# Performance work log

Measured on AMD Instinct MI355X. Metric: run time of the kernel, lower is better.

## Reference

```python
import jax, jax.numpy as jnp
import numpy as np

B, S, D, H, PF = 2, 2048, 1024, 16, 4096
HD = D // H
EPS = 1e-5


def _rope_tables(seq_len, dim, theta=10000.0):
    freqs = 1.0 / (theta ** (np.arange(0, dim, 2)[: dim // 2].astype(np.float32) / dim))
    ang = np.outer(np.arange(seq_len, dtype=np.float32), freqs)  # [S, D/2]
    return jnp.asarray(np.cos(ang)), jnp.asarray(np.sin(ang))


def setup_inputs() -> dict:
    key = jax.random.key(0)
    ks = jax.random.split(key, 16)
    s = 0.02
    inp = {
        "src": jax.random.normal(ks[0], (B, S, D), dtype=jnp.float32),
        "Wq": jax.random.normal(ks[1], (D, D), dtype=jnp.float32) * s,
        "bq": jnp.zeros((D,), jnp.float32),
        "Wk": jax.random.normal(ks[2], (D, D), dtype=jnp.float32) * s,
        "bk": jnp.zeros((D,), jnp.float32),
        "Wv": jax.random.normal(ks[3], (D, D), dtype=jnp.float32) * s,
        "bv": jnp.zeros((D,), jnp.float32),
        "Wo": jax.random.normal(ks[4], (D, D), dtype=jnp.float32) * s,
        "bo": jnp.zeros((D,), jnp.float32),
        "ln1_g": jnp.ones((D,), jnp.float32),
        "ln1_b": jnp.zeros((D,), jnp.float32),
        "W1": jax.random.normal(ks[5], (D, PF), dtype=jnp.float32) * s,
        "b1": jnp.zeros((PF,), jnp.float32),
        "W2": jax.random.normal(ks[6], (PF, D), dtype=jnp.float32) * s,
        "b2": jnp.zeros((D,), jnp.float32),
        "ln2_g": jnp.ones((D,), jnp.float32),
        "ln2_b": jnp.zeros((D,), jnp.float32),
    }
    cos, sin = _rope_tables(S, D)
    inp["rope_cos"] = cos
    inp["rope_sin"] = sin
    return inp


def _apply_rope(x, cos, sin):
    # x: [B, S, D]; rotate adjacent channel pairs as complex numbers (Meta LLaMA style)
    xp = x.reshape(x.shape[0], x.shape[1], -1, 2)
    a, b = xp[..., 0], xp[..., 1]
    c = cos[None, : x.shape[1]]
    s = sin[None, : x.shape[1]]
    out = jnp.stack([a * c - b * s, a * s + b * c], axis=-1)
    return out.reshape(x.shape)


def _layer_norm(x, g, b):
    mu = x.mean(-1, keepdims=True)
    var = ((x - mu) ** 2).mean(-1, keepdims=True)
    return (x - mu) * jax.lax.rsqrt(var + EPS) * g + b


def reference(src, Wq, bq, Wk, bk, Wv, bv, Wo, bo, ln1_g, ln1_b,
              W1, b1, W2, b2, ln2_g, ln2_b, rope_cos, rope_sin):
    bsz, seq, _ = src.shape
    Q = src @ Wq + bq
    K = src @ Wk + bk
    V = src @ Wv + bv
    Q = _apply_rope(Q, rope_cos, rope_sin)
    K = _apply_rope(K, rope_cos, rope_sin)
    # split heads: [B, H, S, HD]
    Q = Q.reshape(bsz, seq, H, HD).transpose(0, 2, 1, 3)
    K = K.reshape(bsz, seq, H, HD).transpose(0, 2, 1, 3)
    V = V.reshape(bsz, seq, H, HD).transpose(0, 2, 1, 3)
    scale = 1.0 / jnp.sqrt(jnp.float32(HD))
    energy = jnp.einsum("bhqd,bhkd->bhqk", Q, K) * scale
    attn = jax.nn.softmax(energy, axis=-1)
    x = jnp.einsum("bhqk,bhkd->bhqd", attn, V)
    x = x.transpose(0, 2, 1, 3).reshape(bsz, seq, D)
    attn_out = x @ Wo + bo
    # residual + LayerNorm
    h = _layer_norm(src + attn_out, ln1_g, ln1_b)
    # positionwise feedforward
    ff = jax.nn.relu(h @ W1 + b1) @ W2 + b2
    return _layer_norm(h + ff, ln2_g, ln2_b)
```

## Files before the change

### kernel.cpp

```cpp
#include <hip/hip_runtime.h>

#define SEQ 2048
#define DIM 1024
#define NH 16
#define HDIM 64
#define PFF 4096
#define NROWS 4096
#define BATCH 2
#define NQKV 3072

typedef unsigned short u16;
typedef unsigned int u32;
typedef __attribute__((ext_vector_type(8))) short short8;
typedef __attribute__((ext_vector_type(4))) float f32x4;
typedef __attribute__((ext_vector_type(16))) float f32x16;

__device__ inline float b2f(u16 u){ return __uint_as_float(((u32)u)<<16); }
__device__ inline u16 f2b(float f){
  u32 u = __float_as_uint(f);
  u32 r = u + 0x7FFFu + ((u>>16)&1u);
  return (u16)(r>>16);
}

#define AS1C(p) ((const __attribute__((address_space(1))) unsigned int*)(p))
#define AS3P(p) ((__attribute__((address_space(3))) unsigned int*)(p))

__global__ void k_cast_bf16(const float* __restrict__ in, u16* __restrict__ out, int n4){
  int i = blockIdx.x*256 + threadIdx.x;
  if (i >= n4) return;
  float4 v = ((const float4*)in)[i];
  ushort4 o;
  o.x = f2b(v.x); o.y = f2b(v.y); o.z = f2b(v.z); o.w = f2b(v.w);
  ((ushort4*)out)[i] = o;
}

__global__ __launch_bounds__(256) void k_transpose_cast(const float* __restrict__ in,
                                                        u16* __restrict__ out, int R, int C){
  __shared__ float tile[32][33];
  int tx = threadIdx.x & 31, ty = threadIdx.x >> 5;
  int c0 = blockIdx.x*32, r0 = blockIdx.y*32;
  #pragma unroll
  for (int i=0;i<4;++i)
    tile[ty+i*8][tx] = in[(size_t)(r0+ty+i*8)*C + c0 + tx];
  __syncthreads();
  #pragma unroll
  for (int i=0;i<4;++i)
    out[(size_t)(c0+ty+i*8)*R + r0 + tx] = f2b(tile[tx][ty+i*8]);
}

__global__ __launch_bounds__(256) void k_transpose_v(const u16* __restrict__ QKV, u16* __restrict__ VT){
  __shared__ u16 tile[32][34];
  int tx = threadIdx.x & 31, ty = threadIdx.x >> 5;
  int d0 = blockIdx.x*32, r0 = blockIdx.y*32;
  #pragma unroll
  for (int i=0;i<4;++i)
    tile[ty+i*8][tx] = QKV[(size_t)(r0+ty+i*8)*NQKV + 2048 + d0 + tx];
  __syncthreads();
  #pragma unroll
  for (int i=0;i<4;++i)
    VT[(size_t)(d0+ty+i*8)*NROWS + r0 + tx] = tile[tx][ty+i*8];
}

__global__ void k_pack3(const float* __restrict__ a, const float* __restrict__ b,
                        const float* __restrict__ c, float* __restrict__ o){
  int i = blockIdx.x*256 + threadIdx.x;
  if (i >= NQKV) return;
  o[i] = i < 1024 ? a[i] : (i < 2048 ? b[i-1024] : c[i-2048]);
}

template<bool RELU, bool BF16OUT, bool BIAS>
__global__ __launch_bounds__(256) void k_gemm(
    const u16* __restrict__ A, const u16* __restrict__ Bt,
    const float* __restrict__ bias, void* __restrict__ Cp,
    int M, int N, int Kc, int lda, int ldb){
  __shared__ __align__(16) char lds[32768];
  const int tid = threadIdx.x;
  const int lane = tid & 63, wid = tid >> 6;
  const int quad = lane >> 4, l15 = lane & 15;
  const int wr = wid >> 1, wc = wid & 1;
  const int nwg = gridDim.x * gridDim.y;
  int lid = blockIdx.y * gridDim.x + blockIdx.x;
  lid = (lid & 7) * (nwg >> 3) + (lid >> 3);
  const int bx = lid % gridDim.x, by = lid / gridDim.x;
  const int rowBase = by * 128, colBase = bx * 128;
  const u16* Az = A  + (size_t)blockIdx.z * Kc;
  const u16* Bz = Bt + (size_t)blockIdx.z * Kc;
  f32x4 acc[4][4] = {};
  const int srow = lane >> 3;
  const int scol = lane & 7;
  for (int k0 = 0; k0 < Kc; k0 += 64) {
    __syncthreads();
    #pragma unroll
    for (int i=0;i<4;++i){
      int wch = wid*4 + i;
      int row = wch*8 + srow;
      int c   = scol ^ (row & 7);
      const u16* ga = Az + (size_t)(rowBase+row)*lda + k0 + c*8;
      __builtin_amdgcn_global_load_lds(AS1C(ga), AS3P(lds + wch*1024), 16, 0, 0);
      const u16* gb = Bz + (size_t)(colBase+row)*ldb + k0 + c*8;
      __builtin_amdgcn_global_load_lds(AS1C(gb), AS3P(lds + 16384 + wch*1024), 16, 0, 0);
    }
    __syncthreads();
    #pragma unroll
    for (int kk=0;kk<2;++kk){
      short8 af[4], bfr[4];
      #pragma unroll
      for (int m=0;m<4;++m){
        int r = wr*64 + m*16 + l15;
        af[m] = *(const short8*)(lds + ((r*128 + kk*64 + quad*16) ^ ((r&7)<<4)));
      }
      #pragma unroll
      for (int n=0;n<4;++n){
        int r = wc*64 + n*16 + l15;
        bfr[n] = *(const short8*)(lds + 16384 + ((r*128 + kk*64 + quad*16) ^ ((r&7)<<4)));
      }
      __builtin_amdgcn_s_setprio(1);
      #pragma unroll
      for (int m=0;m<4;++m)
        #pragma unroll
        for (int n=0;n<4;++n)
          acc[m][n] = __builtin_amdgcn_mfma_f32_16x16x32_bf16(af[m], bfr[n], acc[m][n], 0,0,0);
      __builtin_amdgcn_s_setprio(0);
    }
  }
  float* Cf = (float*)Cp + (size_t)blockIdx.z * M * N;
  #pragma unroll
  for (int m=0;m<4;++m){
    #pragma unroll
    for (int n=0;n<4;++n){
      int col = colBase + wc*64 + n*16 + l15;
      float bv = (BIAS && blockIdx.z == 0) ? bias[col] : 0.f;
      #pragma unroll
      for (int j=0;j<4;++j){
        int row = rowBase + wr*64 + m*16 + quad*4 + j;
        float v = acc[m][n][j] + bv;
        if (RELU) v = fmaxf(v, 0.f);
        if (BF16OUT) ((u16*)Cp)[(size_t)row*N + col] = f2b(v);
        else         Cf[(size_t)row*N + col] = v;
      }
    }
  }
}

__global__ void k_rope(u16* __restrict__ QKV,
                       const float* __restrict__ cosT, const float* __restrict__ sinT){
  int idx = blockIdx.x*256 + threadIdx.x;
  int row = idx >> 9, p = idx & 511;
  int s = row & (SEQ-1);
  float c = cosT[s*512 + p], sn = sinT[s*512 + p];
  u16* qp = QKV + (size_t)row*NQKV + 2*p;
  u16* kp = qp + 1024;
  ushort2 q = *(ushort2*)qp;
  ushort2 k = *(ushort2*)kp;
  float qx = b2f(q.x), qy = b2f(q.y), kx = b2f(k.x), ky = b2f(k.y);
  const float scale = 0.125f;
  ushort2 qo, ko;
  qo.x = f2b((qx*c - qy*sn)*scale);
  qo.y = f2b((qx*sn + qy*c)*scale);
  ko.x = f2b(kx*c - ky*sn);
  ko.y = f2b(kx*sn + ky*c);
  *(ushort2*)qp = qo;
  *(ushort2*)kp = ko;
}

__global__ __launch_bounds__(256) void k_attn(
    const u16* __restrict__ QKV, const u16* __restrict__ VT, u16* __restrict__ Xo){
  const int qt = blockIdx.x, h = blockIdx.y, b = blockIdx.z;
  const int tid = threadIdx.x, lane = tid & 63, wid = tid >> 6;
  const int l31 = lane & 31, hi = lane >> 5;
  __shared__ __align__(16) char lds[32768];
  const int srow = lane >> 3, scol = lane & 7;

  short8 qf[4];
  {
    const u16* qrow = QKV + (size_t)(b*SEQ + qt*128 + wid*32 + l31)*NQKV + h*HDIM;
    #pragma unroll
    for (int dk=0; dk<4; ++dk)
      qf[dk] = *(const short8*)(qrow + dk*16 + 8*hi);
  }
  float m_run = -1e30f, s_run = 0.f;
  f32x16 oacc[2] = {};
  const size_t krow0 = (size_t)(b*SEQ);

  auto do_stage = [&](int buf, int kt){
    char* kdst = lds + buf*16384;
    char* vdst = kdst + 8192;
    #pragma unroll
    for (int i=0;i<2;++i){
      int wch = wid*2 + i;
      int row = wch*8 + srow;
      int c = scol ^ (row & 7);
      const u16* gk = QKV + (krow0 + kt*64 + row)*NQKV + 1024 + h*HDIM + c*8;
      __builtin_amdgcn_global_load_lds(AS1C(gk), AS3P(kdst + wch*1024), 16, 0, 0);
      const u16* gv = VT + (size_t)(h*HDIM + row)*NROWS + b*SEQ + kt*64 + c*8;
      __builtin_amdgcn_global_load_lds(AS1C(gv), AS3P(vdst + wch*1024), 16, 0, 0);
    }
  };

  auto do_tile = [&](int buf){
    char* kb = lds + buf*16384;
    char* vb = kb + 8192;
    f32x16 pacc[2] = {};
    __builtin_amdgcn_s_setprio(1);
    #pragma unroll
    for (int kbk=0;kbk<2;++kbk){
      #pragma unroll
      for (int dk=0;dk<4;++dk){
        int row = kbk*32 + l31;
        short8 kf = *(const short8*)(kb + ((row*128 + dk*32 + 16*hi) ^ ((row&7)<<4)));
        pacc[kbk] = __builtin_amdgcn_mfma_f32_32x32x16_bf16(kf, qf[dk], pacc[kbk], 0,0,0);
      }
    }
    __builtin_amdgcn_s_setprio(0);
    float tmax = -1e30f;
    #pragma unroll
    for (int kbk=0;kbk<2;++kbk)
      #pragma unroll
      for (int r=0;r<16;++r) tmax = fmaxf(tmax, pacc[kbk][r]);
    tmax = fmaxf(tmax, __shfl_xor(tmax, 32));
    if (__any(tmax > m_run + 8.0f)){
      float mnew = fmaxf(m_run, tmax);
      float a = __expf(m_run - mnew);
      s_run *= a;
      m_run = mnew;
      #pragma unroll
      for (int r=0;r<16;++r){
        int src = (r&3) + 8*(r>>2) + 4*hi;
        float ar = __shfl(a, src);
        oacc[0][r] *= ar;
        oacc[1][r] *= ar;
      }
    }
    float p[2][16];
    float psum = 0.f;
    #pragma unroll
    for (int kbk=0;kbk<2;++kbk)
      #pragma unroll
      for (int r=0;r<16;++r){
        float e = __expf(pacc[kbk][r] - m_run);
        p[kbk][r] = e;
        psum += e;
      }
    psum += __shfl_xor(psum, 32);
    s_run += psum;
    short8 pa[4];
    #pragma unroll
    for (int kbk=0;kbk<2;++kbk){
      #pragma unroll
      for (int s=0;s<2;++s){
        u32 X0, X1, Y0, Y1;
        asm("v_cvt_pk_bf16_f32 %0, %1, %2" : "=v"(X0) : "v"(p[kbk][8*s+0]), "v"(p[kbk][8*s+1]));
        asm("v_cvt_pk_bf16_f32 %0, %1, %2" : "=v"(X1) : "v"(p[kbk][8*s+2]), "v"(p[kbk][8*s+3]));
        asm("v_cvt_pk_bf16_f32 %0, %1, %2" : "=v"(Y0) : "v"(p[kbk][8*s+4]), "v"(p[kbk][8*s+5]));
        asm("v_cvt_pk_bf16_f32 %0, %1, %2" : "=v"(Y1) : "v"(p[kbk][8*s+6]), "v"(p[kbk][8*s+7]));
        asm volatile("v_permlane32_swap_b32 %0, %1" : "+v"(X0), "+v"(Y0));
        asm volatile("v_permlane32_swap_b32 %0, %1" : "+v"(X1), "+v"(Y1));
        union { u32 w[4]; short8 s8; } pu;
        pu.w[0] = X0; pu.w[1] = X1; pu.w[2] = Y0; pu.w[3] = Y1;
        pa[2*kbk+s] = pu.s8;
      }
    }
    __builtin_amdgcn_s_setprio(1);
    #pragma unroll
    for (int db=0;db<2;++db){
      #pragma unroll
      for (int ks=0;ks<4;++ks){
        int row = db*32 + l31;
        short8 vf = *(const short8*)(vb + ((row*128 + ks*32 + 16*hi) ^ ((row&7)<<4)));
        oacc[db] = __builtin_amdgcn_mfma_f32_32x32x16_bf16(pa[ks], vf, oacc[db], 0,0,0);
      }
    }
    __builtin_amdgcn_s_setprio(0);
  };

  do_stage(0, 0);
  __syncthreads();
  const int NT = SEQ/64;
  #pragma unroll 1
  for (int kt=0; kt<NT; kt+=2){
    do_stage(1, kt+1);
    do_tile(0);
    __syncthreads();
    if (kt+2 < NT) do_stage(0, kt+2);
    do_tile(1);
    __syncthreads();
  }
  #pragma unroll
  for (int r=0;r<16;++r){
    int crow = (r&3) + 8*(r>>2) + 4*hi;
    float sq = __shfl(s_run, crow);
    float rs = __builtin_amdgcn_rcpf(sq);
    int grow = b*SEQ + qt*128 + wid*32 + crow;
    Xo[(size_t)grow*DIM + h*HDIM + l31]      = f2b(oacc[0][r] * rs);
    Xo[(size_t)grow*DIM + h*HDIM + 32 + l31] = f2b(oacc[1][r] * rs);
  }
}

template<int PARTS, bool WBF>
__global__ __launch_bounds__(256) void k_ln(
    const float* __restrict__ a, const float* __restrict__ p0, const float* __restrict__ p1,
    const float* __restrict__ p2, const float* __restrict__ p3,
    const float* __restrict__ g, const float* __restrict__ be,
    float* __restrict__ outf, u16* __restrict__ outb){
  const int row = blockIdx.x, tid = threadIdx.x;
  __shared__ float red[8];
  float4 av = ((const float4*)(a  + (size_t)row*DIM))[tid];
  float4 b0 = ((const float4*)(p0 + (size_t)row*DIM))[tid];
  float4 b1 = ((const float4*)(p1 + (size_t)row*DIM))[tid];
  float x0 = av.x+b0.x+b1.x, x1 = av.y+b0.y+b1.y, x2 = av.z+b0.z+b1.z, x3 = av.w+b0.w+b1.w;
  if constexpr (PARTS == 4){
    float4 b2v = ((const float4*)(p2 + (size_t)row*DIM))[tid];
    float4 b3v = ((const float4*)(p3 + (size_t)row*DIM))[tid];
    x0 += b2v.x+b3v.x; x1 += b2v.y+b3v.y; x2 += b2v.z+b3v.z; x3 += b2v.w+b3v.w;
  }
  float s = x0+x1+x2+x3;
  #pragma unroll
  for (int o=32;o>=1;o>>=1) s += __shfl_down(s, o);
  if ((tid&63)==0) red[tid>>6] = s;
  __syncthreads();
  float mean = (red[0]+red[1]+red[2]+red[3]) * (1.0f/DIM);
  float d0=x0-mean, d1=x1-mean, d2=x2-mean, d3=x3-mean;
  float vs = d0*d0+d1*d1+d2*d2+d3*d3;
  #pragma unroll
  for (int o=32;o>=1;o>>=1) vs += __shfl_down(vs, o);
  if ((tid&63)==0) red[4+(tid>>6)] = vs;
  __syncthreads();
  float var = (red[4]+red[5]+red[6]+red[7]) * (1.0f/DIM);
  float rs = rsqrtf(var + 1e-5f);
  float4 gv = ((const float4*)g)[tid];
  float4 bev = ((const float4*)be)[tid];
  float4 y;
  y.x = d0*rs*gv.x + bev.x;
  y.y = d1*rs*gv.y + bev.y;
  y.z = d2*rs*gv.z + bev.z;
  y.w = d3*rs*gv.w + bev.w;
  ((float4*)(outf + (size_t)row*DIM))[tid] = y;
  if (WBF){
    ushort4 o4; o4.x=f2b(y.x); o4.y=f2b(y.y); o4.z=f2b(y.z); o4.w=f2b(y.w);
    ((ushort4*)(outb + (size_t)row*DIM))[tid] = o4;
  }
}

extern "C" void kernel_launch(void* const* d_in, const int* in_sizes, int n_in,
                              void* d_out, int out_size, void* d_ws, size_t ws_size,
                              hipStream_t stream){
  (void)in_sizes; (void)n_in; (void)out_size; (void)ws_size;
  const float* src  = (const float*)d_in[0];
  const float* Wq   = (const float*)d_in[1];
  const float* bq   = (const float*)d_in[2];
  const float* Wk   = (const float*)d_in[3];
  const float* bk   = (const float*)d_in[4];
  const float* Wv   = (const float*)d_in[5];
  const float* bv   = (const float*)d_in[6];
  const float* Wo   = (const float*)d_in[7];
  const float* bo   = (const float*)d_in[8];
  const float* ln1g = (const float*)d_in[9];
  const float* ln1b = (const float*)d_in[10];
  const float* W1   = (const float*)d_in[11];
  const float* b1   = (const float*)d_in[12];
  const float* W2   = (const float*)d_in[13];
  const float* b2   = (const float*)d_in[14];
  const float* ln2g = (const float*)d_in[15];
  const float* ln2b = (const float*)d_in[16];
  const float* rc   = (const float*)d_in[17];
  const float* rsn  = (const float*)d_in[18];

  char* ws = (char*)d_ws;
  const size_t MB = (size_t)1<<20;
  u16* Xbf   = (u16*)(ws);
  u16* QKV   = (u16*)(ws + 8*MB);
  u16* VTb   = (u16*)(ws + 32*MB);
  float* aop   = (float*)(ws + 8*MB);
  float* ff2p  = (float*)(ws + 8*MB);
  u16* xat   = (u16*)(ws + 40*MB);
  u16* hbf   = (u16*)(ws + 48*MB);
  u16* WqkvT = (u16*)(ws + 56*MB);
  u16* WoT   = (u16*)(ws + 62*MB);
  u16* W1T   = (u16*)(ws + 64*MB);
  u16* W2T   = (u16*)(ws + 72*MB);
  u16* ff1   = (u16*)(ws + 80*MB);
  float* h   = (float*)(ws + 112*MB);
  float* bqkv= (float*)(ws + 128*MB);
  const size_t P16 = 16*MB/4;

  dim3 blk(256);
  k_cast_bf16<<<dim3(NROWS*DIM/1024), blk, 0, stream>>>(src, Xbf, NROWS*DIM/4);
  k_transpose_cast<<<dim3(DIM/32, DIM/32), blk, 0, stream>>>(Wq, WqkvT, DIM, DIM);
  k_transpose_cast<<<dim3(DIM/32, DIM/32), blk, 0, stream>>>(Wk, WqkvT + (size_t)1024*1024, DIM, DIM);
  k_transpose_cast<<<dim3(DIM/32, DIM/32), blk, 0, stream>>>(Wv, WqkvT + (size_t)2048*1024, DIM, DIM);
  k_transpose_cast<<<dim3(DIM/32, DIM/32), blk, 0, stream>>>(Wo, WoT, DIM, DIM);
  k_transpose_cast<<<dim3(PFF/32, DIM/32), blk, 0, stream>>>(W1, W1T, DIM, PFF);
  k_transpose_cast<<<dim3(DIM/32, PFF/32), blk, 0, stream>>>(W2, W2T, PFF, DIM);
  k_pack3<<<dim3(12), blk, 0, stream>>>(bq, bk, bv, bqkv);

  k_gemm<false,true,true><<<dim3(NQKV/128, NROWS/128), blk, 0, stream>>>(
      Xbf, WqkvT, bqkv, QKV, NROWS, NQKV, DIM, DIM, DIM);
  k_rope<<<dim3(NROWS*512/256), blk, 0, stream>>>(QKV, rc, rsn);
  k_transpose_v<<<dim3(DIM/32, NROWS/32), blk, 0, stream>>>(QKV, VTb);
  k_attn<<<dim3(SEQ/128, NH, BATCH), blk, 0, stream>>>(QKV, VTb, xat);
  k_gemm<false,false,true><<<dim3(DIM/128, NROWS/128, 2), blk, 0, stream>>>(
      xat, WoT, bo, aop, NROWS, DIM, 512, DIM, DIM);
  k_ln<2,true><<<dim3(NROWS), blk, 0, stream>>>(src, aop, aop + P16, nullptr, nullptr,
                                                ln1g, ln1b, h, hbf);
  k_gemm<true,true,true><<<dim3(PFF/128, NROWS/128), blk, 0, stream>>>(
      hbf, W1T, b1, ff1, NROWS, PFF, DIM, DIM, DIM);
  k_gemm<false,false,true><<<dim3(DIM/128, NROWS/128, 2), blk, 0, stream>>>(
      ff1, W2T, b2, ff2p, NROWS, DIM, 2048, PFF, PFF);
  k_ln<2,false><<<dim3(NROWS), blk, 0, stream>>>(h, ff2p, ff2p + P16, nullptr, nullptr,
                                                 ln2g, ln2b, (float*)d_out, nullptr);
}
```

Measured before the change: 265.9 us.

## Add 256x256-tile 8-wave GEMM with ping-pong LDS pipeline for QKV and FFN1

```diff
diff --git a/kernel.cpp b/kernel.cpp
--- a/kernel.cpp
+++ b/kernel.cpp
@@ -66,6 +66,140 @@
   int i = blockIdx.x*256 + threadIdx.x;
   if (i >= NQKV) return;
   o[i] = i < 1024 ? a[i] : (i < 2048 ? b[i-1024] : c[i-2048]);
+}
+
+template<bool RELU, bool BF16OUT>
+__global__ __launch_bounds__(512, 2) void k_gemm256(
+    const u16* __restrict__ A, const u16* __restrict__ Bt,
+    const float* __restrict__ bias, void* __restrict__ Cp,
+    int M, int N, int K, int lda, int ldb){
+  extern __shared__ char lds[];
+  const int tid = threadIdx.x;
+  const int lane = tid & 63, wid = tid >> 6;
+  const int quad = lane >> 4, l15 = lane & 15;
+  const int wm = wid >> 2, wn = wid & 3;
+  const int ro = (l15*4 + quad)*16;
+  const int srow = lane >> 2;
+  const int sk   = (lane & 3)*8;
+  const int nwg = gridDim.x * gridDim.y;
+  int lid = blockIdx.y * gridDim.x + blockIdx.x;
+  lid = (lid & 7) * (nwg >> 3) + (lid >> 3);
+  const int bx = lid % gridDim.x, by = lid / gridDim.x;
+  const int rowBase = by*256, colBase = bx*256;
+
+  f32x4 acc[8][4] = {};
+
+  auto stage2 = [&](int buf, int k0, int i){
+    int idx = i*8 + wid;
+    int rs = idx >> 1, ks = idx & 1;
+    const u16* ga = A + (size_t)(rowBase + rs*16 + srow)*lda + k0 + ks*32 + sk;
+    __builtin_amdgcn_global_load_lds(AS1C(ga), AS3P(lds + buf*65536 + idx*1024), 16, 0, 0);
+    const u16* gb = Bt + (size_t)(colBase + rs*16 + srow)*ldb + k0 + ks*32 + sk;
+    __builtin_amdgcn_global_load_lds(AS1C(gb), AS3P(lds + buf*65536 + 32768 + idx*1024), 16, 0, 0);
+  };
+
+  #pragma unroll
+  for (int i=0;i<4;++i) stage2(0, 0, i);
+  __syncthreads();
+
+  const int NT = K >> 6;
+  #pragma unroll 1
+  for (int t=0; t<NT; ++t){
+    const int buf = t & 1;
+    const bool pf = (t+1 < NT);
+    const int k0n = (t+1)*64;
+    char* Ab = lds + buf*65536;
+    char* Bb = Ab + 32768;
+    short8 a0[4][2], a1[4][2], b0[2][2], b1[2][2];
+
+    #pragma unroll
+    for (int mf=0; mf<4; ++mf)
+      #pragma unroll
+      for (int kk=0; kk<2; ++kk)
+        a0[mf][kk] = *(const short8*)(Ab + ((wm*8+mf)*2+kk)*1024 + ro);
+    #pragma unroll
+    for (int nf=0; nf<2; ++nf)
+      #pragma unroll
+      for (int kk=0; kk<2; ++kk)
+        b0[nf][kk] = *(const short8*)(Bb + ((wn*4+nf)*2+kk)*1024 + ro);
+    if (pf){ stage2(buf^1, k0n, 0); stage2(buf^1, k0n, 1); }
+    __builtin_amdgcn_s_barrier();
+    __builtin_amdgcn_s_setprio(1);
+    #pragma unroll
+    for (int mf=0; mf<4; ++mf)
+      #pragma unroll
+      for (int nf=0; nf<2; ++nf)
+        #pragma unroll
+        for (int kk=0; kk<2; ++kk)
+          acc[mf][nf] = __builtin_amdgcn_mfma_f32_16x16x32_bf16(a0[mf][kk], b0[nf][kk], acc[mf][nf], 0,0,0);
+    __builtin_amdgcn_s_setprio(0);
+    __builtin_amdgcn_s_barrier();
+
+    #pragma unroll
+    for (int nf=0; nf<2; ++nf)
+      #pragma unroll
+      for (int kk=0; kk<2; ++kk)
+        b1[nf][kk] = *(const short8*)(Bb + ((wn*4+2+nf)*2+kk)*1024 + ro);
+    if (pf){ stage2(buf^1, k0n, 2); stage2(buf^1, k0n, 3); }
+    __builtin_amdgcn_s_barrier();
+    __builtin_amdgcn_s_setprio(1);
+    #pragma unroll
+    for (int mf=0; mf<4; ++mf)
+      #pragma unroll
+      for (int nf=0; nf<2; ++nf)
+        #pragma unroll
+        for (int kk=0; kk<2; ++kk)
+          acc[mf][2+nf] = __builtin_amdgcn_mfma_f32_16x16x32_bf16(a0[mf][kk], b1[nf][kk], acc[mf][2+nf], 0,0,0);
+    __builtin_amdgcn_s_setprio(0);
+    __builtin_amdgcn_s_barrier();
+
+    #pragma unroll
+    for (int mf=0; mf<4; ++mf)
+      #pragma unroll
+      for (int kk=0; kk<2; ++kk)
+        a1[mf][kk] = *(const short8*)(Ab + ((wm*8+4+mf)*2+kk)*1024 + ro);
+    __builtin_amdgcn_s_barrier();
+    __builtin_amdgcn_s_setprio(1);
+    #pragma unroll
+    for (int mf=0; mf<4; ++mf)
+      #pragma unroll
+      for (int nf=0; nf<2; ++nf)
+        #pragma unroll
+        for (int kk=0; kk<2; ++kk)
+          acc[4+mf][2+nf] = __builtin_amdgcn_mfma_f32_16x16x32_bf16(a1[mf][kk], b1[nf][kk], acc[4+mf][2+nf], 0,0,0);
+    __builtin_amdgcn_s_setprio(0);
+    __builtin_amdgcn_s_barrier();
+
+    if (pf) asm volatile("s_waitcnt vmcnt(0)" ::: "memory");
+    __builtin_amdgcn_s_barrier();
+    __builtin_amdgcn_s_setprio(1);
+    #pragma unroll
+    for (int mf=0; mf<4; ++mf)
+      #pragma unroll
+      for (int nf=0; nf<2; ++nf)
+        #pragma unroll
+        for (int kk=0; kk<2; ++kk)
+          acc[4+mf][nf] = __builtin_amdgcn_mfma_f32_16x16x32_bf16(a1[mf][kk], b0[nf][kk], acc[4+mf][nf], 0,0,0);
+    __builtin_amdgcn_s_setprio(0);
+    __builtin_amdgcn_s_barrier();
+  }
+
+  #pragma unroll
+  for (int mf=0; mf<8; ++mf){
+    #pragma unroll
+    for (int nf=0; nf<4; ++nf){
+      int col = colBase + wn*64 + nf*16 + l15;
+      float bv = bias[col];
+      #pragma unroll
+      for (int j=0; j<4; ++j){
+        int row = rowBase + wm*128 + mf*16 + quad*4 + j;
+        float v = acc[mf][nf][j] + bv;
+        if (RELU) v = fmaxf(v, 0.f);
+        if (BF16OUT) ((u16*)Cp)[(size_t)row*N + col] = f2b(v);
+        else         ((float*)Cp)[(size_t)row*N + col] = v;
+      }
+    }
+  }
 }
 
 template<bool RELU, bool BF16OUT, bool BIAS>
@@ -299,7 +433,6 @@
 template<int PARTS, bool WBF>
 __global__ __launch_bounds__(256) void k_ln(
     const float* __restrict__ a, const float* __restrict__ p0, const float* __restrict__ p1,
-    const float* __restrict__ p2, const float* __restrict__ p3,
     const float* __restrict__ g, const float* __restrict__ be,
     float* __restrict__ outf, u16* __restrict__ outb){
   const int row = blockIdx.x, tid = threadIdx.x;
@@ -308,11 +441,6 @@
   float4 b0 = ((const float4*)(p0 + (size_t)row*DIM))[tid];
   float4 b1 = ((const float4*)(p1 + (size_t)row*DIM))[tid];
   float x0 = av.x+b0.x+b1.x, x1 = av.y+b0.y+b1.y, x2 = av.z+b0.z+b1.z, x3 = av.w+b0.w+b1.w;
-  if constexpr (PARTS == 4){
-    float4 b2v = ((const float4*)(p2 + (size_t)row*DIM))[tid];
-    float4 b3v = ((const float4*)(p3 + (size_t)row*DIM))[tid];
-    x0 += b2v.x+b3v.x; x1 += b2v.y+b3v.y; x2 += b2v.z+b3v.z; x3 += b2v.w+b3v.w;
-  }
   float s = x0+x1+x2+x3;
   #pragma unroll
   for (int o=32;o>=1;o>>=1) s += __shfl_down(s, o);
@@ -383,6 +511,11 @@
   float* bqkv= (float*)(ws + 128*MB);
   const size_t P16 = 16*MB/4;
 
+  hipFuncSetAttribute((const void*)&k_gemm256<false,true>,
+                      hipFuncAttributeMaxDynamicSharedMemorySize, 131072);
+  hipFuncSetAttribute((const void*)&k_gemm256<true,true>,
+                      hipFuncAttributeMaxDynamicSharedMemorySize, 131072);
+
   dim3 blk(256);
   k_cast_bf16<<<dim3(NROWS*DIM/1024), blk, 0, stream>>>(src, Xbf, NROWS*DIM/4);
   k_transpose_cast<<<dim3(DIM/32, DIM/32), blk, 0, stream>>>(Wq, WqkvT, DIM, DIM);
@@ -393,19 +526,17 @@
   k_transpose_cast<<<dim3(DIM/32, PFF/32), blk, 0, stream>>>(W2, W2T, PFF, DIM);
   k_pack3<<<dim3(12), blk, 0, stream>>>(bq, bk, bv, bqkv);
 
-  k_gemm<false,true,true><<<dim3(NQKV/128, NROWS/128), blk, 0, stream>>>(
+  k_gemm256<false,true><<<dim3(NQKV/256, NROWS/256), dim3(512), 131072, stream>>>(
       Xbf, WqkvT, bqkv, QKV, NROWS, NQKV, DIM, DIM, DIM);
   k_rope<<<dim3(NROWS*512/256), blk, 0, stream>>>(QKV, rc, rsn);
   k_transpose_v<<<dim3(DIM/32, NROWS/32), blk, 0, stream>>>(QKV, VTb);
   k_attn<<<dim3(SEQ/128, NH, BATCH), blk, 0, stream>>>(QKV, VTb, xat);
   k_gemm<false,false,true><<<dim3(DIM/128, NROWS/128, 2), blk, 0, stream>>>(
       xat, WoT, bo, aop, NROWS, DIM, 512, DIM, DIM);
-  k_ln<2,true><<<dim3(NROWS), blk, 0, stream>>>(src, aop, aop + P16, nullptr, nullptr,
-                                                ln1g, ln1b, h, hbf);
-  k_gemm<true,true,true><<<dim3(PFF/128, NROWS/128), blk, 0, stream>>>(
+  k_ln<2,true><<<dim3(NROWS), blk, 0, stream>>>(src, aop, aop + P16, ln1g, ln1b, h, hbf);
+  k_gemm256<true,true><<<dim3(PFF/256, NROWS/256), dim3(512), 131072, stream>>>(
       hbf, W1T, b1, ff1, NROWS, PFF, DIM, DIM, DIM);
   k_gemm<false,false,true><<<dim3(DIM/128, NROWS/128, 2), blk, 0, stream>>>(
       ff1, W2T, b2, ff2p, NROWS, DIM, 2048, PFF, PFF);
-  k_ln<2,false><<<dim3(NROWS), blk, 0, stream>>>(h, ff2p, ff2p + P16, nullptr, nullptr,
-                                                 ln2g, ln2b, (float*)d_out, nullptr);
-}
+  k_ln<2,false><<<dim3(NROWS), blk, 0, stream>>>(h, ff2p, ff2p + P16, ln2g, ln2b, (float*)d_out, nullptr);
+}
```

After: 255.4 us. 1.04x faster.
